# Kernel optimization log

Measured on AMD Instinct MI355X. Metric: run time of the kernel, lower is better.

The kernel has to match this reference:

```python
import jax, jax.numpy as jnp
import numpy as np

C = 64
DQ = C // 8  # query/key channel dim


def setup_inputs() -> dict:
    key = jax.random.key(0)
    ks = jax.random.split(key, 8)
    B, H, W = 8, 64, 64
    x = jax.random.normal(ks[0], (B, C, H, W), dtype=jnp.float32)
    # 1x1 conv weights stored as [out, in] matrices (kernel dims squeezed)
    wq = jax.random.normal(ks[1], (DQ, C), dtype=jnp.float32) * 0.05
    bq = jax.random.normal(ks[2], (DQ,), dtype=jnp.float32) * 0.05
    wk = jax.random.normal(ks[3], (DQ, C), dtype=jnp.float32) * 0.05
    bk = jax.random.normal(ks[4], (DQ,), dtype=jnp.float32) * 0.05
    wv = jax.random.normal(ks[5], (C, C), dtype=jnp.float32) * 0.05
    bv = jax.random.normal(ks[6], (C,), dtype=jnp.float32) * 0.05
    gamma = jax.random.normal(ks[7], (1,), dtype=jnp.float32)
    return {"x": x, "wq": wq, "bq": bq, "wk": wk, "bk": bk,
            "wv": wv, "bv": bv, "gamma": gamma}


def reference(x, wq, bq, wk, bk, wv, bv, gamma):
    B, Cc, H, W = x.shape
    N = H * W
    xf = x.reshape(B, Cc, N)                      # [B, C, N]
    # 1x1 convs == channel matmuls
    q = jnp.einsum('dc,bcn->bdn', wq, xf) + bq[None, :, None]   # [B, DQ, N]
    k = jnp.einsum('dc,bcn->bdn', wk, xf) + bk[None, :, None]   # [B, DQ, N]
    v = jnp.einsum('oc,bcn->bon', wv, xf) + bv[None, :, None]   # [B, C, N]
    # energy[b, m, n] = sum_d q[b, d, m] * k[b, d, n]
    energy = jnp.einsum('bdm,bdn->bmn', q, k)                   # [B, N, N]
    attention = jax.nn.softmax(energy, axis=-1)
    # out[b, c, m] = sum_n v[b, c, n] * attention[b, m, n]
    out = jnp.einsum('bcn,bmn->bcm', v, attention).reshape(B, Cc, H, W)
    return gamma[0] * out + x
```

## Files before the change

kernel.cpp:

```cpp
#include <hip/hip_runtime.h>
#include <math.h>

#define NTOK 4096
#define CCH  64

typedef __attribute__((ext_vector_type(8)))  short bf16x8;
typedef __attribute__((ext_vector_type(4)))  float f32x4;
typedef __attribute__((ext_vector_type(16))) float f32x16;
typedef __attribute__((ext_vector_type(2)))  unsigned int uint32x2;

__device__ __forceinline__ unsigned short f2bf_rne(float f) {
    unsigned int u = __float_as_uint(f);
    u += 0x7FFFu + ((u >> 16) & 1u);
    return (unsigned short)(u >> 16);
}
__device__ __forceinline__ unsigned short f2bf_trunc(float f) {
    return (unsigned short)(__float_as_uint(f) >> 16);
}

__global__ __launch_bounds__(256) void proj_kernel(
    const float* __restrict__ x,
    const float* __restrict__ wq, const float* __restrict__ bq,
    const float* __restrict__ wk, const float* __restrict__ bk,
    const float* __restrict__ wv, const float* __restrict__ bv,
    unsigned short* __restrict__ qt, unsigned short* __restrict__ kt,
    unsigned short* __restrict__ vbf)
{
    __shared__ float xs[64 * 68];
    __shared__ float wvs[64 * 65];
    __shared__ float wqs[8 * 64];
    __shared__ float wks[8 * 64];
    __shared__ float bvs[64];
    __shared__ float bqs[8];
    __shared__ float bks[8];
    __shared__ unsigned short vtmp[64 * 66];

    const int t  = threadIdx.x;
    const int b  = blockIdx.x >> 6;
    const int n0 = (blockIdx.x & 63) << 6;

    {
        const int nloc = t & 63;
        const int r0   = t >> 6;
        #pragma unroll
        for (int r = 0; r < 16; ++r) {
            const int c = r0 + r * 4;
            xs[c * 68 + nloc] = x[((size_t)b * 64 + c) * NTOK + n0 + nloc];
        }
    }
    #pragma unroll
    for (int r = 0; r < 16; ++r) {
        const int i = t + 256 * r;
        wvs[(i >> 6) * 65 + (i & 63)] = wv[i];
    }
    wqs[t]       = wq[t];
    wqs[t + 256] = wq[t + 256];
    wks[t]       = wk[t];
    wks[t + 256] = wk[t + 256];
    if (t < 64)  bvs[t] = bv[t];
    if (t < 8)   { bqs[t] = bq[t]; bks[t] = bk[t]; }
    __syncthreads();

    {
        const int c  = t & 63;
        const int nr = t >> 6;
        float acc[16];
        #pragma unroll
        for (int i = 0; i < 16; ++i) acc[i] = bvs[c];
        const float* xbase = &xs[nr * 16];
        for (int cp = 0; cp < 64; ++cp) {
            const float w = wvs[c * 65 + cp];
            const float* xrow = &xbase[cp * 68];
            #pragma unroll
            for (int i = 0; i < 16; ++i) acc[i] += w * xrow[i];
        }
        #pragma unroll
        for (int i = 0; i < 16; ++i)
            vtmp[c * 66 + 4 * i + nr] = f2bf_rne(acc[i]);
    }

    {
        const int nn  = t & 63;
        const int sel = t >> 6;
        const int d0  = (sel & 1) * 4;
        const float* ws = (sel & 2) ? wks : wqs;
        const float* bs = (sel & 2) ? bks : bqs;
        float acc[4];
        #pragma unroll
        for (int j = 0; j < 4; ++j) acc[j] = bs[d0 + j];
        for (int cp = 0; cp < 64; ++cp) {
            const float xv = xs[cp * 68 + nn];
            #pragma unroll
            for (int j = 0; j < 4; ++j) acc[j] += ws[(d0 + j) * 64 + cp] * xv;
        }
        const unsigned int lo = (unsigned int)f2bf_rne(acc[0]) |
                                ((unsigned int)f2bf_rne(acc[1]) << 16);
        const unsigned int hi = (unsigned int)f2bf_rne(acc[2]) |
                                ((unsigned int)f2bf_rne(acc[3]) << 16);
        unsigned short* dst = ((sel & 2) ? kt : qt) +
                              ((size_t)(b * NTOK + n0 + nn)) * 8 + d0;
        *(uint32x2*)dst = (uint32x2){lo, hi};
    }
    __syncthreads();

    {
        const int c = t >> 2;
        const int q = t & 3;
        unsigned short* dst = vbf + ((size_t)(b * CCH + c)) * NTOK + n0 + q * 16;
        *(bf16x8*)dst       = *(const bf16x8*)&vtmp[c * 66 + q * 16];
        *(bf16x8*)(dst + 8) = *(const bf16x8*)&vtmp[c * 66 + q * 16 + 8];
    }
}

__global__ __launch_bounds__(256) void attn_kernel(
    const unsigned short* __restrict__ qt, const unsigned short* __restrict__ kt,
    const unsigned short* __restrict__ vbf,
    const float* __restrict__ x, const float* __restrict__ gamma_p,
    float* __restrict__ out)
{
    __shared__ unsigned short qs[64 * 32];
    __shared__ unsigned short ks[64 * 40];
    __shared__ unsigned short vs[64 * 88];
    __shared__ unsigned short ps[64 * 88];
    __shared__ float          ls[64];

    const int t    = threadIdx.x;
    const int lane = t & 63;
    const int w    = t >> 6;
    const int b    = blockIdx.x >> 6;
    const int m0   = (blockIdx.x & 63) << 6;

    const int l15 = lane & 15;
    const int g   = lane >> 4;
    const int l31 = lane & 31;
    const int h   = lane >> 5;

    if (t < 64) {
        *(bf16x8*)&qs[t * 32] = *(const bf16x8*)&qt[((size_t)(b * NTOK + m0 + t)) * 8];
        bf16x8 z = {};
        *(bf16x8*)&qs[t * 32 + 8]  = z;
        *(bf16x8*)&qs[t * 32 + 16] = z;
        *(bf16x8*)&qs[t * 32 + 24] = z;
        *(bf16x8*)&ks[t * 40 + 8]  = z;
        *(bf16x8*)&ks[t * 40 + 16] = z;
        *(bf16x8*)&ks[t * 40 + 24] = z;
    }
    __syncthreads();

    const bf16x8 a_q = *(const bf16x8*)&qs[(w * 16 + l15) * 32 + g * 8];

    f32x16 oacc;
    #pragma unroll
    for (int i = 0; i < 16; ++i) oacc[i] = 0.f;
    float rs0 = 0.f, rs1 = 0.f, rs2 = 0.f, rs3 = 0.f;

    const int crow = ((w >> 1) * 32 + l31) * 88;
    const int mrow = ((w & 1) * 32 + l31) * 88;

    for (int it = 0; it < 64; ++it) {
        const int nt0 = it << 6;
        __syncthreads();

        if (t < 64)
            *(bf16x8*)&ks[t * 40] = *(const bf16x8*)&kt[((size_t)(b * NTOK + nt0 + t)) * 8];
        #pragma unroll
        for (int r = 0; r < 2; ++r) {
            const int i   = t + 256 * r;
            const int c   = i >> 3;
            const int seg = i & 7;
            *(bf16x8*)&vs[c * 88 + seg * 8] =
                *(const bf16x8*)&vbf[((size_t)(b * CCH + c)) * NTOK + nt0 + seg * 8];
        }
        __syncthreads();

        f32x4 s0, s1, s2, s3;
        {
            const bf16x8 bk0 = *(const bf16x8*)&ks[( 0 + l15) * 40 + g * 8];
            const bf16x8 bk1 = *(const bf16x8*)&ks[(16 + l15) * 40 + g * 8];
            const bf16x8 bk2 = *(const bf16x8*)&ks[(32 + l15) * 40 + g * 8];
            const bf16x8 bk3 = *(const bf16x8*)&ks[(48 + l15) * 40 + g * 8];
            const f32x4 z = {0.f, 0.f, 0.f, 0.f};
            s0 = __builtin_amdgcn_mfma_f32_16x16x32_bf16(a_q, bk0, z, 0, 0, 0);
            s1 = __builtin_amdgcn_mfma_f32_16x16x32_bf16(a_q, bk1, z, 0, 0, 0);
            s2 = __builtin_amdgcn_mfma_f32_16x16x32_bf16(a_q, bk2, z, 0, 0, 0);
            s3 = __builtin_amdgcn_mfma_f32_16x16x32_bf16(a_q, bk3, z, 0, 0, 0);
        }

        #pragma unroll
        for (int r = 0; r < 4; ++r) {
            const float p0 = __expf(s0[r]);
            const float p1 = __expf(s1[r]);
            const float p2 = __expf(s2[r]);
            const float p3 = __expf(s3[r]);
            const unsigned int lo = (unsigned int)f2bf_trunc(p0) |
                                    ((unsigned int)f2bf_trunc(p1) << 16);
            const unsigned int hi = (unsigned int)f2bf_trunc(p2) |
                                    ((unsigned int)f2bf_trunc(p3) << 16);
            *(uint32x2*)&ps[(w * 16 + g * 4 + r) * 88 + 4 * l15] = (uint32x2){lo, hi};
            const float ssum = (p0 + p1) + (p2 + p3);
            if      (r == 0) rs0 += ssum;
            else if (r == 1) rs1 += ssum;
            else if (r == 2) rs2 += ssum;
            else             rs3 += ssum;
        }
        __syncthreads();

        #pragma unroll
        for (int kc = 0; kc < 4; ++kc) {
            const bf16x8 a_v = *(const bf16x8*)&vs[crow + kc * 16 + h * 8];
            const bf16x8 b_p = *(const bf16x8*)&ps[mrow + kc * 16 + h * 8];
            oacc = __builtin_amdgcn_mfma_f32_32x32x16_bf16(a_v, b_p, oacc, 0, 0, 0);
        }
    }

    #pragma unroll
    for (int xm = 1; xm <= 8; xm <<= 1) {
        rs0 += __shfl_xor(rs0, xm);
        rs1 += __shfl_xor(rs1, xm);
        rs2 += __shfl_xor(rs2, xm);
        rs3 += __shfl_xor(rs3, xm);
    }
    if (l15 == 0) {
        ls[w * 16 + g * 4 + 0] = rs0;
        ls[w * 16 + g * 4 + 1] = rs1;
        ls[w * 16 + g * 4 + 2] = rs2;
        ls[w * 16 + g * 4 + 3] = rs3;
    }
    __syncthreads();

    {
        const int mloc = (w & 1) * 32 + l31;
        const float sc = gamma_p[0] / ls[mloc];
        #pragma unroll
        for (int reg = 0; reg < 16; ++reg) {
            const int c = (w >> 1) * 32 + (reg & 3) + 8 * (reg >> 2) + 4 * h;
            const size_t idx = ((size_t)(b * CCH + c)) * NTOK + m0 + mloc;
            out[idx] = oacc[reg] * sc + x[idx];
        }
    }
}

extern "C" void kernel_launch(void* const* d_in, const int* in_sizes, int n_in,
                              void* d_out, int out_size, void* d_ws, size_t ws_size,
                              hipStream_t stream) {
    const float* x     = (const float*)d_in[0];
    const float* wq    = (const float*)d_in[1];
    const float* bq    = (const float*)d_in[2];
    const float* wk    = (const float*)d_in[3];
    const float* bk    = (const float*)d_in[4];
    const float* wv    = (const float*)d_in[5];
    const float* bv    = (const float*)d_in[6];
    const float* gamma = (const float*)d_in[7];
    float* out = (float*)d_out;

    const int B = in_sizes[0] / (CCH * NTOK);

    unsigned short* ws  = (unsigned short*)d_ws;
    unsigned short* qt  = ws;
    unsigned short* kt  = qt + (size_t)B * NTOK * 8;
    unsigned short* vbf = kt + (size_t)B * NTOK * 8;

    const int nTiles = NTOK / 64;
    proj_kernel<<<B * nTiles, 256, 0, stream>>>(x, wq, bq, wk, bk, wv, bv,
                                                qt, kt, vbf);
    attn_kernel<<<B * nTiles, 256, 0, stream>>>(qt, kt, vbf, x, gamma, out);
}
```

Baseline: 151.4 us.

## Split attention over key halves, MFMA projections, exp2 softmax with combine pass

```diff
diff --git a/kernel.cpp b/kernel.cpp
--- a/kernel.cpp
+++ b/kernel.cpp
@@ -3,6 +3,7 @@
 
 #define NTOK 4096
 #define CCH  64
+#define LOG2E 1.4426950408889634f
 
 typedef __attribute__((ext_vector_type(8)))  short bf16x8;
 typedef __attribute__((ext_vector_type(4)))  float f32x4;
@@ -16,6 +17,9 @@
 }
 __device__ __forceinline__ unsigned short f2bf_trunc(float f) {
     return (unsigned short)(__float_as_uint(f) >> 16);
+}
+__device__ __forceinline__ float bf2f(unsigned short u) {
+    return __uint_as_float(((unsigned int)u) << 16);
 }
 
 __global__ __launch_bounds__(256) void proj_kernel(
@@ -26,79 +30,81 @@
     unsigned short* __restrict__ qt, unsigned short* __restrict__ kt,
     unsigned short* __restrict__ vbf)
 {
-    __shared__ float xs[64 * 68];
-    __shared__ float wvs[64 * 65];
-    __shared__ float wqs[8 * 64];
-    __shared__ float wks[8 * 64];
-    __shared__ float bvs[64];
-    __shared__ float bqs[8];
-    __shared__ float bks[8];
+    __shared__ unsigned short xsb[64 * 68];
+    __shared__ unsigned short wa[80 * 68];
     __shared__ unsigned short vtmp[64 * 66];
+    __shared__ float bb[80];
 
     const int t  = threadIdx.x;
     const int b  = blockIdx.x >> 6;
     const int n0 = (blockIdx.x & 63) << 6;
 
-    {
-        const int nloc = t & 63;
-        const int r0   = t >> 6;
+    const int lane = t & 63;
+    const int w    = t >> 6;
+    const int l15  = lane & 15;
+    const int g    = lane >> 4;
+
+    {
+        const int n  = t & 63;
+        const int c0 = t >> 6;
         #pragma unroll
         for (int r = 0; r < 16; ++r) {
-            const int c = r0 + r * 4;
-            xs[c * 68 + nloc] = x[((size_t)b * 64 + c) * NTOK + n0 + nloc];
+            const int c = c0 + 4 * r;
+            xsb[n * 68 + c] = f2bf_rne(x[((size_t)(b * CCH + c)) * NTOK + n0 + n]);
         }
     }
     #pragma unroll
     for (int r = 0; r < 16; ++r) {
         const int i = t + 256 * r;
-        wvs[(i >> 6) * 65 + (i & 63)] = wv[i];
-    }
-    wqs[t]       = wq[t];
-    wqs[t + 256] = wq[t + 256];
-    wks[t]       = wk[t];
-    wks[t + 256] = wk[t + 256];
-    if (t < 64)  bvs[t] = bv[t];
-    if (t < 8)   { bqs[t] = bq[t]; bks[t] = bk[t]; }
+        wa[(i >> 6) * 68 + (i & 63)] = f2bf_rne(wv[i]);
+    }
+    {
+        const int i0 = t, i1 = t + 256;
+        wa[(64 + (i0 >> 6)) * 68 + (i0 & 63)] = f2bf_rne(wq[i0] * LOG2E);
+        wa[(64 + (i1 >> 6)) * 68 + (i1 & 63)] = f2bf_rne(wq[i1] * LOG2E);
+        wa[(72 + (i0 >> 6)) * 68 + (i0 & 63)] = f2bf_rne(wk[i0]);
+        wa[(72 + (i1 >> 6)) * 68 + (i1 & 63)] = f2bf_rne(wk[i1]);
+    }
+    if (t < 80) {
+        float bias;
+        if (t < 64)      bias = bv[t];
+        else if (t < 72) bias = bq[t - 64] * LOG2E;
+        else             bias = bk[t - 72];
+        bb[t] = bias;
+    }
     __syncthreads();
 
-    {
-        const int c  = t & 63;
-        const int nr = t >> 6;
-        float acc[16];
-        #pragma unroll
-        for (int i = 0; i < 16; ++i) acc[i] = bvs[c];
-        const float* xbase = &xs[nr * 16];
-        for (int cp = 0; cp < 64; ++cp) {
-            const float w = wvs[c * 65 + cp];
-            const float* xrow = &xbase[cp * 68];
-            #pragma unroll
-            for (int i = 0; i < 16; ++i) acc[i] += w * xrow[i];
-        }
-        #pragma unroll
-        for (int i = 0; i < 16; ++i)
-            vtmp[c * 66 + 4 * i + nr] = f2bf_rne(acc[i]);
-    }
-
-    {
-        const int nn  = t & 63;
-        const int sel = t >> 6;
-        const int d0  = (sel & 1) * 4;
-        const float* ws = (sel & 2) ? wks : wqs;
-        const float* bs = (sel & 2) ? bks : bqs;
-        float acc[4];
-        #pragma unroll
-        for (int j = 0; j < 4; ++j) acc[j] = bs[d0 + j];
-        for (int cp = 0; cp < 64; ++cp) {
-            const float xv = xs[cp * 68 + nn];
-            #pragma unroll
-            for (int j = 0; j < 4; ++j) acc[j] += ws[(d0 + j) * 64 + cp] * xv;
-        }
-        const unsigned int lo = (unsigned int)f2bf_rne(acc[0]) |
-                                ((unsigned int)f2bf_rne(acc[1]) << 16);
-        const unsigned int hi = (unsigned int)f2bf_rne(acc[2]) |
-                                ((unsigned int)f2bf_rne(acc[3]) << 16);
-        unsigned short* dst = ((sel & 2) ? kt : qt) +
-                              ((size_t)(b * NTOK + n0 + nn)) * 8 + d0;
+    f32x4 acc[5];
+    #pragma unroll
+    for (int mt = 0; mt < 5; ++mt) acc[mt] = (f32x4){0.f, 0.f, 0.f, 0.f};
+    #pragma unroll
+    for (int kc = 0; kc < 2; ++kc) {
+        const bf16x8 bx = *(const bf16x8*)&xsb[(w * 16 + l15) * 68 + kc * 32 + g * 8];
+        #pragma unroll
+        for (int mt = 0; mt < 5; ++mt) {
+            const bf16x8 aw = *(const bf16x8*)&wa[(mt * 16 + l15) * 68 + kc * 32 + g * 8];
+            acc[mt] = __builtin_amdgcn_mfma_f32_16x16x32_bf16(aw, bx, acc[mt], 0, 0, 0);
+        }
+    }
+
+    const int n = w * 16 + l15;
+    #pragma unroll
+    for (int mt = 0; mt < 4; ++mt) {
+        #pragma unroll
+        for (int r = 0; r < 4; ++r) {
+            const int c = mt * 16 + g * 4 + r;
+            vtmp[c * 66 + 4 * l15 + w] = f2bf_rne(acc[mt][r] + bb[c]);
+        }
+    }
+    {
+        unsigned short vals[4];
+        #pragma unroll
+        for (int r = 0; r < 4; ++r)
+            vals[r] = f2bf_rne(acc[4][r] + bb[64 + g * 4 + r]);
+        const unsigned int lo = (unsigned int)vals[0] | ((unsigned int)vals[1] << 16);
+        const unsigned int hi = (unsigned int)vals[2] | ((unsigned int)vals[3] << 16);
+        unsigned short* dst = ((g < 2) ? qt : kt) +
+                              ((size_t)(b * NTOK + n0 + n)) * 8 + (g & 1) * 4;
         *(uint32x2*)dst = (uint32x2){lo, hi};
     }
     __syncthreads();
@@ -112,23 +118,23 @@
     }
 }
 
-__global__ __launch_bounds__(256) void attn_kernel(
+__global__ __launch_bounds__(256, 4) void attn_kernel(
     const unsigned short* __restrict__ qt, const unsigned short* __restrict__ kt,
     const unsigned short* __restrict__ vbf,
-    const float* __restrict__ x, const float* __restrict__ gamma_p,
-    float* __restrict__ out)
+    unsigned short* __restrict__ opart, float* __restrict__ lpart)
 {
     __shared__ unsigned short qs[64 * 32];
     __shared__ unsigned short ks[64 * 40];
     __shared__ unsigned short vs[64 * 88];
     __shared__ unsigned short ps[64 * 88];
-    __shared__ float          ls[64];
 
     const int t    = threadIdx.x;
     const int lane = t & 63;
     const int w    = t >> 6;
-    const int b    = blockIdx.x >> 6;
-    const int m0   = (blockIdx.x & 63) << 6;
+    const int p    = blockIdx.x >> 9;
+    const int rest = blockIdx.x & 511;
+    const int b    = rest >> 6;
+    const int m0   = (rest & 63) << 6;
 
     const int l15 = lane & 15;
     const int g   = lane >> 4;
@@ -157,7 +163,7 @@
     const int crow = ((w >> 1) * 32 + l31) * 88;
     const int mrow = ((w & 1) * 32 + l31) * 88;
 
-    for (int it = 0; it < 64; ++it) {
+    for (int it = p * 32; it < p * 32 + 32; ++it) {
         const int nt0 = it << 6;
         __syncthreads();
 
@@ -188,10 +194,10 @@
 
         #pragma unroll
         for (int r = 0; r < 4; ++r) {
-            const float p0 = __expf(s0[r]);
-            const float p1 = __expf(s1[r]);
-            const float p2 = __expf(s2[r]);
-            const float p3 = __expf(s3[r]);
+            const float p0 = exp2f(s0[r]);
+            const float p1 = exp2f(s1[r]);
+            const float p2 = exp2f(s2[r]);
+            const float p3 = exp2f(s3[r]);
             const unsigned int lo = (unsigned int)f2bf_trunc(p0) |
                                     ((unsigned int)f2bf_trunc(p1) << 16);
             const unsigned int hi = (unsigned int)f2bf_trunc(p2) |
@@ -221,23 +227,47 @@
         rs3 += __shfl_xor(rs3, xm);
     }
     if (l15 == 0) {
-        ls[w * 16 + g * 4 + 0] = rs0;
-        ls[w * 16 + g * 4 + 1] = rs1;
-        ls[w * 16 + g * 4 + 2] = rs2;
-        ls[w * 16 + g * 4 + 3] = rs3;
-    }
-    __syncthreads();
+        float* lp = lpart + (size_t)(p * 8 + b) * NTOK + m0 + w * 16 + g * 4;
+        lp[0] = rs0; lp[1] = rs1; lp[2] = rs2; lp[3] = rs3;
+    }
 
     {
         const int mloc = (w & 1) * 32 + l31;
-        const float sc = gamma_p[0] / ls[mloc];
         #pragma unroll
         for (int reg = 0; reg < 16; ++reg) {
             const int c = (w >> 1) * 32 + (reg & 3) + 8 * (reg >> 2) + 4 * h;
-            const size_t idx = ((size_t)(b * CCH + c)) * NTOK + m0 + mloc;
-            out[idx] = oacc[reg] * sc + x[idx];
-        }
-    }
+            opart[((size_t)((p * 8 + b) * CCH + c)) * NTOK + m0 + mloc] =
+                f2bf_rne(oacc[reg]);
+        }
+    }
+}
+
+__global__ __launch_bounds__(256) void combine_kernel(
+    const unsigned short* __restrict__ opart, const float* __restrict__ lpart,
+    const float* __restrict__ x, const float* __restrict__ gamma_p,
+    float* __restrict__ out)
+{
+    const size_t idx = (size_t)blockIdx.x * 256 + threadIdx.x;
+    const int m4 = ((int)idx & 1023) * 4;
+    const int bc = (int)(idx >> 10);
+    const int bi = bc >> 6;
+
+    const size_t obase   = (size_t)bc * NTOK + m4;
+    const size_t ostride = (size_t)8 * CCH * NTOK;
+
+    const ushort4 o1 = *(const ushort4*)&opart[obase];
+    const ushort4 o2 = *(const ushort4*)&opart[obase + ostride];
+    const float4  l1 = *(const float4*)&lpart[(size_t)bi * NTOK + m4];
+    const float4  l2 = *(const float4*)&lpart[(size_t)(8 + bi) * NTOK + m4];
+    const float4  xv = *(const float4*)&x[obase];
+    const float   gm = gamma_p[0];
+
+    float4 r;
+    r.x = (bf2f(o1.x) + bf2f(o2.x)) * gm / (l1.x + l2.x) + xv.x;
+    r.y = (bf2f(o1.y) + bf2f(o2.y)) * gm / (l1.y + l2.y) + xv.y;
+    r.z = (bf2f(o1.z) + bf2f(o2.z)) * gm / (l1.z + l2.z) + xv.z;
+    r.w = (bf2f(o1.w) + bf2f(o2.w)) * gm / (l1.w + l2.w) + xv.w;
+    *(float4*)&out[obase] = r;
 }
 
 extern "C" void kernel_launch(void* const* d_in, const int* in_sizes, int n_in,
@@ -255,13 +285,16 @@
 
     const int B = in_sizes[0] / (CCH * NTOK);
 
-    unsigned short* ws  = (unsigned short*)d_ws;
-    unsigned short* qt  = ws;
-    unsigned short* kt  = qt + (size_t)B * NTOK * 8;
-    unsigned short* vbf = kt + (size_t)B * NTOK * 8;
-
-    const int nTiles = NTOK / 64;
-    proj_kernel<<<B * nTiles, 256, 0, stream>>>(x, wq, bq, wk, bk, wv, bv,
-                                                qt, kt, vbf);
-    attn_kernel<<<B * nTiles, 256, 0, stream>>>(qt, kt, vbf, x, gamma, out);
-}
+    unsigned short* wsp   = (unsigned short*)d_ws;
+    unsigned short* qt    = wsp;
+    unsigned short* kt    = qt + (size_t)B * NTOK * 8;
+    unsigned short* vbf   = kt + (size_t)B * NTOK * 8;
+    unsigned short* opart = vbf + (size_t)B * CCH * NTOK;
+    float*          lpart = (float*)(opart + (size_t)2 * B * CCH * NTOK);
+
+    proj_kernel<<<B * (NTOK / 64), 256, 0, stream>>>(x, wq, bq, wk, bk, wv, bv,
+                                                     qt, kt, vbf);
+    attn_kernel<<<2 * B * (NTOK / 64), 256, 0, stream>>>(qt, kt, vbf, opart, lpart);
+    combine_kernel<<<(B * CCH * NTOK) / (256 * 4), 256, 0, stream>>>(
+        opart, lpart, x, gamma, out);
+}
```

After: 135.7 us. -10.4%, faster.
